# Optimization experiments

Hardware: AMD Instinct MI355X
Metric: run time of the kernel (lower is better)

Reference implementation:

```python
import jax, jax.numpy as jnp
import numpy as np

B, C, T = 8, 1025, 3000


def setup_inputs() -> dict:
    key = jax.random.key(0)
    k1, k2 = jax.random.split(key)
    x_real = jax.random.normal(k1, (B, C, T), dtype=jnp.float32)
    x_imag = jax.random.normal(k2, (B, C, T), dtype=jnp.float32)
    return {"x_real": x_real, "x_imag": x_imag}


def reference(x_real, x_imag):
    # coherent_polar: magnitude + min-max-normalized unwrapped phase, cat on channel dim
    magnitude = jnp.sqrt(x_real * x_real + x_imag * x_imag)  # torch.abs(complex)
    phase = jnp.arctan2(x_imag, x_real)                      # torch.angle

    pi = jnp.float32(np.pi)
    two_pi = jnp.float32(2.0 * np.pi)

    phase_diff = phase[:, :, 1:] - phase[:, :, :-1]          # [B, C, T-1]
    # per-step correction: +2pi where diff < -pi, -2pi where diff > pi
    steps = jnp.where(phase_diff < -pi, two_pi, jnp.float32(0.0)) \
          + jnp.where(phase_diff > pi, -two_pi, jnp.float32(0.0))
    # the original sequential loop is an inclusive prefix-sum of the steps
    correction = jnp.concatenate(
        [jnp.zeros_like(phase[:, :, :1]), jnp.cumsum(steps, axis=2)], axis=2
    )  # [B, C, T]

    unwrapped = phase + correction
    phase_min = jnp.min(unwrapped, axis=2, keepdims=True)
    phase_max = jnp.max(unwrapped, axis=2, keepdims=True)
    phase_norm = (unwrapped - phase_min) / (phase_max - phase_min + 1e-8)

    return jnp.concatenate([magnitude, phase_norm], axis=1)  # [B, 2C, T]
```

## Files before the change

### kernel.cpp

```cpp
#include <hip/hip_runtime.h>

namespace {
constexpr int kB = 8;
constexpr int kC = 1025;
constexpr int kT = 3000;
constexpr int kThreads = 256;
constexpr int kWaves = kThreads / 64;
constexpr int kSeg = kThreads * 4;
constexpr int kNSeg = 3;
constexpr float kPi = 3.14159265358979323846f;
constexpr float kTwoPi = 6.28318530717958647692f;
constexpr float kPiO2 = 1.57079632679489661923f;
}

typedef float v4f __attribute__((ext_vector_type(4)));
typedef float v2f __attribute__((ext_vector_type(2)));

__device__ __forceinline__ v2f atan_core2(v2f t) {
  const v2f s = t * t;
  v2f p = v2f{0.00282363896258175373f, 0.00282363896258175373f};
  p = p * s + v2f{-0.0159569028764963150f, -0.0159569028764963150f};
  p = p * s + v2f{0.0425049886107444763f, 0.0425049886107444763f};
  p = p * s + v2f{-0.0748900920152664185f, -0.0748900920152664185f};
  p = p * s + v2f{0.106347933411598206f, 0.106347933411598206f};
  p = p * s + v2f{-0.142027363181114197f, -0.142027363181114197f};
  p = p * s + v2f{0.199926957488059998f, 0.199926957488059998f};
  p = p * s + v2f{-0.333331018686294556f, -0.333331018686294556f};
  return (p * s) * t + t;
}

__device__ __forceinline__ void fast_atan2_4(const v4f y4, const v4f x4,
                                             float out[4]) {
  float t[4], ax[4], ay[4];
  const float xs[4] = {x4.x, x4.y, x4.z, x4.w};
  const float ys[4] = {y4.x, y4.y, y4.z, y4.w};
#pragma unroll
  for (int k = 0; k < 4; ++k) {
    ax[k] = __builtin_fabsf(xs[k]);
    ay[k] = __builtin_fabsf(ys[k]);
    const float mx = fmaxf(ax[k], ay[k]);
    const float mn = fminf(ax[k], ay[k]);
    float tt = mn * __builtin_amdgcn_rcpf(mx);
    if (mx == 0.0f) tt = 0.0f;
    t[k] = tt;
  }
  const v2f a01 = atan_core2(v2f{t[0], t[1]});
  const v2f a23 = atan_core2(v2f{t[2], t[3]});
  const float av[4] = {a01.x, a01.y, a23.x, a23.y};
#pragma unroll
  for (int k = 0; k < 4; ++k) {
    float a = av[k];
    a = (ay[k] > ax[k]) ? (kPiO2 - a) : a;
    a = (xs[k] < 0.0f) ? (kPi - a) : a;
    out[k] = copysignf(a, ys[k]);
  }
}

__global__ __launch_bounds__(kThreads, 8) void coherent_polar_kernel(
    const float* __restrict__ xr, const float* __restrict__ xi,
    float* __restrict__ out) {
  __shared__ float s_last[kNSeg][kThreads];
  __shared__ float s_wsum[kWaves][kNSeg];
  __shared__ float s_wmin[kWaves][kNSeg];
  __shared__ float s_wmax[kWaves][kNSeg];

  const int row = blockIdx.x;
  const int b = row / kC;
  const int c = row - b * kC;
  const float* re = xr + (size_t)row * kT;
  const float* im = xi + (size_t)row * kT;
  float* mag_out = out + ((size_t)b * (2 * kC) + c) * kT;
  float* ph_out  = out + ((size_t)b * (2 * kC) + kC + c) * kT;

  const int tid = threadIdx.x;
  const int lane = tid & 63;
  const int wave = tid >> 6;

  bool act[kNSeg];
  int offs[kNSeg];
#pragma unroll
  for (int s = 0; s < kNSeg; ++s) {
    offs[s] = s * kSeg + tid * 4;
    act[s] = offs[s] < kT;
  }

  v4f r4[kNSeg], i4[kNSeg];
#pragma unroll
  for (int s = 0; s < kNSeg; ++s) {
    if (act[s]) {
      r4[s] = *reinterpret_cast<const v4f*>(re + offs[s]);
      i4[s] = *reinterpret_cast<const v4f*>(im + offs[s]);
    }
  }

  float ph[kNSeg][4];
#pragma unroll
  for (int s = 0; s < kNSeg; ++s) {
    if (act[s]) {
      v4f m4;
      m4.x = __builtin_amdgcn_sqrtf(fmaf(r4[s].x, r4[s].x, i4[s].x * i4[s].x));
      m4.y = __builtin_amdgcn_sqrtf(fmaf(r4[s].y, r4[s].y, i4[s].y * i4[s].y));
      m4.z = __builtin_amdgcn_sqrtf(fmaf(r4[s].z, r4[s].z, i4[s].z * i4[s].z));
      m4.w = __builtin_amdgcn_sqrtf(fmaf(r4[s].w, r4[s].w, i4[s].w * i4[s].w));
      *reinterpret_cast<v4f*>(mag_out + offs[s]) = m4;
      fast_atan2_4(i4[s], r4[s], ph[s]);
    }
  }

#pragma unroll
  for (int s = 0; s < kNSeg; ++s) s_last[s][tid] = act[s] ? ph[s][3] : 0.0f;
  __syncthreads();
  float prevph[kNSeg];
#pragma unroll
  for (int s = 0; s < kNSeg; ++s) {
    if (tid > 0)       prevph[s] = s_last[s][tid - 1];
    else if (s > 0)    prevph[s] = s_last[s - 1][kThreads - 1];
    else               prevph[s] = ph[0][0];
  }

  float T[kNSeg];
#pragma unroll
  for (int s = 0; s < kNSeg; ++s) {
    float run = 0.0f;
    if (act[s]) {
      float p = prevph[s];
#pragma unroll
      for (int k = 0; k < 4; ++k) {
        const float cur = ph[s][k];
        const float d = cur - p;
        p = cur;
        float step = 0.0f;
        if (d < -kPi) step = kTwoPi;
        else if (d > kPi) step = -kTwoPi;
        run += step;
        ph[s][k] = cur + run;
      }
    }
    T[s] = act[s] ? run : 0.0f;
  }

  float inc[kNSeg] = {T[0], T[1], T[2]};
#pragma unroll
  for (int d = 1; d < 64; d <<= 1) {
#pragma unroll
    for (int s = 0; s < kNSeg; ++s) {
      const float n = __shfl_up(inc[s], d);
      if (lane >= d) inc[s] += n;
    }
  }
  float excl[kNSeg];
#pragma unroll
  for (int s = 0; s < kNSeg; ++s) excl[s] = inc[s] - T[s];

  float mn[kNSeg], mx[kNSeg];
#pragma unroll
  for (int s = 0; s < kNSeg; ++s) {
    mn[s] = __builtin_inff();
    mx[s] = -__builtin_inff();
    if (act[s]) {
#pragma unroll
      for (int k = 0; k < 4; ++k) {
        const float u = ph[s][k] + excl[s];
        mn[s] = fminf(mn[s], u);
        mx[s] = fmaxf(mx[s], u);
      }
    }
  }
#pragma unroll
  for (int m = 32; m >= 1; m >>= 1) {
#pragma unroll
    for (int s = 0; s < kNSeg; ++s) {
      mn[s] = fminf(mn[s], __shfl_xor(mn[s], m));
      mx[s] = fmaxf(mx[s], __shfl_xor(mx[s], m));
    }
  }
  if (lane == 63) {
#pragma unroll
    for (int s = 0; s < kNSeg; ++s) s_wsum[wave][s] = inc[s];
  }
  if (lane == 0) {
#pragma unroll
    for (int s = 0; s < kNSeg; ++s) { s_wmin[wave][s] = mn[s]; s_wmax[wave][s] = mx[s]; }
  }
  __syncthreads();

  float wavePref[kWaves][kNSeg];
  float blockTot[kNSeg];
#pragma unroll
  for (int s = 0; s < kNSeg; ++s) {
    float acc = 0.0f;
#pragma unroll
    for (int w = 0; w < kWaves; ++w) { wavePref[w][s] = acc; acc += s_wsum[w][s]; }
    blockTot[s] = acc;
  }
  float segBase[kNSeg];
  segBase[0] = 0.0f;
  segBase[1] = blockTot[0];
  segBase[2] = blockTot[0] + blockTot[1];

  float gmn = __builtin_inff();
  float gmx = -__builtin_inff();
#pragma unroll
  for (int w = 0; w < kWaves; ++w) {
#pragma unroll
    for (int s = 0; s < kNSeg; ++s) {
      const float off = segBase[s] + wavePref[w][s];
      gmn = fminf(gmn, s_wmin[w][s] + off);
      gmx = fmaxf(gmx, s_wmax[w][s] + off);
    }
  }
  const float inv = 1.0f / (gmx - gmn + 1e-8f);

#pragma unroll
  for (int s = 0; s < kNSeg; ++s) {
    if (act[s]) {
      const float base = segBase[s] + wavePref[wave][s] + excl[s] - gmn;
      v4f o;
      o.x = (ph[s][0] + base) * inv;
      o.y = (ph[s][1] + base) * inv;
      o.z = (ph[s][2] + base) * inv;
      o.w = (ph[s][3] + base) * inv;
      *reinterpret_cast<v4f*>(ph_out + offs[s]) = o;
    }
  }
}

extern "C" void kernel_launch(void* const* d_in, const int* in_sizes, int n_in,
                              void* d_out, int out_size, void* d_ws, size_t ws_size,
                              hipStream_t stream) {
  const float* xr = (const float*)d_in[0];
  const float* xi = (const float*)d_in[1];
  float* out = (float*)d_out;
  coherent_polar_kernel<<<dim3(kB * kC), dim3(kThreads), 0, stream>>>(xr, xi, out);
}
```

Baseline: 80.21 us.

## Process four rows per block with register prefetch of next row

Switches from one block per row to a grid of 2050 blocks, each looping over four rows with a stride of 2050. The next row's real and imaginary data is loaded into registers while the current row's scan and normalization run, so global loads overlap with compute. Output stores become nontemporal, and __syncthreads is replaced by a custom LDS wait plus barrier. The costs are higher register pressure, reflected in launch bounds lowered from 8 to 4 blocks, and fewer concurrent blocks.

```diff
diff --git a/kernel.cpp b/kernel.cpp
--- a/kernel.cpp
+++ b/kernel.cpp
@@ -3,11 +3,14 @@
 namespace {
 constexpr int kB = 8;
 constexpr int kC = 1025;
+constexpr int kRows = kB * kC;
 constexpr int kT = 3000;
 constexpr int kThreads = 256;
 constexpr int kWaves = kThreads / 64;
 constexpr int kSeg = kThreads * 4;
 constexpr int kNSeg = 3;
+constexpr int kGridB = 2050;
+constexpr int kRowsPer = 4;
 constexpr float kPi = 3.14159265358979323846f;
 constexpr float kTwoPi = 6.28318530717958647692f;
 constexpr float kPiO2 = 1.57079632679489661923f;
@@ -15,6 +18,12 @@
 
 typedef float v4f __attribute__((ext_vector_type(4)));
 typedef float v2f __attribute__((ext_vector_type(2)));
+
+__device__ __forceinline__ void sync_lds() {
+  asm volatile("s_waitcnt lgkmcnt(0)" ::: "memory");
+  __builtin_amdgcn_s_barrier();
+  asm volatile("" ::: "memory");
+}
 
 __device__ __forceinline__ v2f atan_core2(v2f t) {
   const v2f s = t * t;
@@ -56,7 +65,20 @@
   }
 }
 
-__global__ __launch_bounds__(kThreads, 8) void coherent_polar_kernel(
+__device__ __forceinline__ void load_row(const float* __restrict__ re,
+                                         const float* __restrict__ im,
+                                         int tid, v4f r4[kNSeg], v4f i4[kNSeg]) {
+#pragma unroll
+  for (int s = 0; s < kNSeg; ++s) {
+    const int off = s * kSeg + tid * 4;
+    if (s < 2 || off < kT) {
+      r4[s] = *reinterpret_cast<const v4f*>(re + off);
+      i4[s] = *reinterpret_cast<const v4f*>(im + off);
+    }
+  }
+}
+
+__global__ __launch_bounds__(kThreads, 4) void coherent_polar_kernel(
     const float* __restrict__ xr, const float* __restrict__ xi,
     float* __restrict__ out) {
   __shared__ float s_last[kNSeg][kThreads];
@@ -64,163 +86,163 @@
   __shared__ float s_wmin[kWaves][kNSeg];
   __shared__ float s_wmax[kWaves][kNSeg];
 
-  const int row = blockIdx.x;
-  const int b = row / kC;
-  const int c = row - b * kC;
-  const float* re = xr + (size_t)row * kT;
-  const float* im = xi + (size_t)row * kT;
-  float* mag_out = out + ((size_t)b * (2 * kC) + c) * kT;
-  float* ph_out  = out + ((size_t)b * (2 * kC) + kC + c) * kT;
-
+  const int bid = blockIdx.x;
   const int tid = threadIdx.x;
   const int lane = tid & 63;
   const int wave = tid >> 6;
-
-  bool act[kNSeg];
-  int offs[kNSeg];
-#pragma unroll
-  for (int s = 0; s < kNSeg; ++s) {
-    offs[s] = s * kSeg + tid * 4;
-    act[s] = offs[s] < kT;
-  }
-
-  v4f r4[kNSeg], i4[kNSeg];
-#pragma unroll
-  for (int s = 0; s < kNSeg; ++s) {
-    if (act[s]) {
-      r4[s] = *reinterpret_cast<const v4f*>(re + offs[s]);
-      i4[s] = *reinterpret_cast<const v4f*>(im + offs[s]);
-    }
-  }
-
-  float ph[kNSeg][4];
-#pragma unroll
-  for (int s = 0; s < kNSeg; ++s) {
-    if (act[s]) {
-      v4f m4;
-      m4.x = __builtin_amdgcn_sqrtf(fmaf(r4[s].x, r4[s].x, i4[s].x * i4[s].x));
-      m4.y = __builtin_amdgcn_sqrtf(fmaf(r4[s].y, r4[s].y, i4[s].y * i4[s].y));
-      m4.z = __builtin_amdgcn_sqrtf(fmaf(r4[s].z, r4[s].z, i4[s].z * i4[s].z));
-      m4.w = __builtin_amdgcn_sqrtf(fmaf(r4[s].w, r4[s].w, i4[s].w * i4[s].w));
-      *reinterpret_cast<v4f*>(mag_out + offs[s]) = m4;
-      fast_atan2_4(i4[s], r4[s], ph[s]);
-    }
-  }
-
-#pragma unroll
-  for (int s = 0; s < kNSeg; ++s) s_last[s][tid] = act[s] ? ph[s][3] : 0.0f;
-  __syncthreads();
-  float prevph[kNSeg];
-#pragma unroll
-  for (int s = 0; s < kNSeg; ++s) {
-    if (tid > 0)       prevph[s] = s_last[s][tid - 1];
-    else if (s > 0)    prevph[s] = s_last[s - 1][kThreads - 1];
-    else               prevph[s] = ph[0][0];
-  }
-
-  float T[kNSeg];
-#pragma unroll
-  for (int s = 0; s < kNSeg; ++s) {
-    float run = 0.0f;
-    if (act[s]) {
-      float p = prevph[s];
-#pragma unroll
-      for (int k = 0; k < 4; ++k) {
-        const float cur = ph[s][k];
-        const float d = cur - p;
-        p = cur;
-        float step = 0.0f;
-        if (d < -kPi) step = kTwoPi;
-        else if (d > kPi) step = -kTwoPi;
-        run += step;
-        ph[s][k] = cur + run;
-      }
-    }
-    T[s] = act[s] ? run : 0.0f;
-  }
-
-  float inc[kNSeg] = {T[0], T[1], T[2]};
-#pragma unroll
-  for (int d = 1; d < 64; d <<= 1) {
-#pragma unroll
-    for (int s = 0; s < kNSeg; ++s) {
-      const float n = __shfl_up(inc[s], d);
-      if (lane >= d) inc[s] += n;
-    }
-  }
-  float excl[kNSeg];
-#pragma unroll
-  for (int s = 0; s < kNSeg; ++s) excl[s] = inc[s] - T[s];
-
-  float mn[kNSeg], mx[kNSeg];
-#pragma unroll
-  for (int s = 0; s < kNSeg; ++s) {
-    mn[s] = __builtin_inff();
-    mx[s] = -__builtin_inff();
-    if (act[s]) {
-#pragma unroll
-      for (int k = 0; k < 4; ++k) {
-        const float u = ph[s][k] + excl[s];
-        mn[s] = fminf(mn[s], u);
-        mx[s] = fmaxf(mx[s], u);
-      }
-    }
-  }
-#pragma unroll
-  for (int m = 32; m >= 1; m >>= 1) {
-#pragma unroll
-    for (int s = 0; s < kNSeg; ++s) {
-      mn[s] = fminf(mn[s], __shfl_xor(mn[s], m));
-      mx[s] = fmaxf(mx[s], __shfl_xor(mx[s], m));
-    }
-  }
-  if (lane == 63) {
-#pragma unroll
-    for (int s = 0; s < kNSeg; ++s) s_wsum[wave][s] = inc[s];
-  }
-  if (lane == 0) {
-#pragma unroll
-    for (int s = 0; s < kNSeg; ++s) { s_wmin[wave][s] = mn[s]; s_wmax[wave][s] = mx[s]; }
-  }
-  __syncthreads();
-
-  float wavePref[kWaves][kNSeg];
-  float blockTot[kNSeg];
-#pragma unroll
-  for (int s = 0; s < kNSeg; ++s) {
-    float acc = 0.0f;
-#pragma unroll
-    for (int w = 0; w < kWaves; ++w) { wavePref[w][s] = acc; acc += s_wsum[w][s]; }
-    blockTot[s] = acc;
-  }
-  float segBase[kNSeg];
-  segBase[0] = 0.0f;
-  segBase[1] = blockTot[0];
-  segBase[2] = blockTot[0] + blockTot[1];
-
-  float gmn = __builtin_inff();
-  float gmx = -__builtin_inff();
-#pragma unroll
-  for (int w = 0; w < kWaves; ++w) {
-#pragma unroll
-    for (int s = 0; s < kNSeg; ++s) {
-      const float off = segBase[s] + wavePref[w][s];
-      gmn = fminf(gmn, s_wmin[w][s] + off);
-      gmx = fmaxf(gmx, s_wmax[w][s] + off);
-    }
-  }
-  const float inv = 1.0f / (gmx - gmn + 1e-8f);
-
-#pragma unroll
-  for (int s = 0; s < kNSeg; ++s) {
-    if (act[s]) {
-      const float base = segBase[s] + wavePref[wave][s] + excl[s] - gmn;
-      v4f o;
-      o.x = (ph[s][0] + base) * inv;
-      o.y = (ph[s][1] + base) * inv;
-      o.z = (ph[s][2] + base) * inv;
-      o.w = (ph[s][3] + base) * inv;
-      *reinterpret_cast<v4f*>(ph_out + offs[s]) = o;
+  const bool act2 = tid * 4 + 2 * kSeg < kT;
+
+  v4f r4[kNSeg], i4[kNSeg], r4n[kNSeg], i4n[kNSeg];
+  load_row(xr + (size_t)bid * kT, xi + (size_t)bid * kT, tid, r4, i4);
+
+#pragma unroll 1
+  for (int r = 0; r < kRowsPer; ++r) {
+    const int row = bid + r * kGridB;
+    const int b = row / kC;
+    const int c = row - b * kC;
+    float* mag_out = out + ((size_t)b * (2 * kC) + c) * kT;
+    float* ph_out  = out + ((size_t)b * (2 * kC) + kC + c) * kT;
+
+    float ph[kNSeg][4];
+#pragma unroll
+    for (int s = 0; s < kNSeg; ++s) {
+      if (s < 2 || act2) {
+        v4f m4;
+        m4.x = __builtin_amdgcn_sqrtf(fmaf(r4[s].x, r4[s].x, i4[s].x * i4[s].x));
+        m4.y = __builtin_amdgcn_sqrtf(fmaf(r4[s].y, r4[s].y, i4[s].y * i4[s].y));
+        m4.z = __builtin_amdgcn_sqrtf(fmaf(r4[s].z, r4[s].z, i4[s].z * i4[s].z));
+        m4.w = __builtin_amdgcn_sqrtf(fmaf(r4[s].w, r4[s].w, i4[s].w * i4[s].w));
+        __builtin_nontemporal_store(m4, reinterpret_cast<v4f*>(mag_out + s * kSeg + tid * 4));
+        fast_atan2_4(i4[s], r4[s], ph[s]);
+      }
+    }
+
+    if (r + 1 < kRowsPer) {
+      const int nrow = row + kGridB;
+      load_row(xr + (size_t)nrow * kT, xi + (size_t)nrow * kT, tid, r4n, i4n);
+    }
+
+#pragma unroll
+    for (int s = 0; s < kNSeg; ++s)
+      s_last[s][tid] = (s < 2 || act2) ? ph[s][3] : 0.0f;
+    sync_lds();
+    float prevph[kNSeg];
+#pragma unroll
+    for (int s = 0; s < kNSeg; ++s) {
+      if (tid > 0)       prevph[s] = s_last[s][tid - 1];
+      else if (s > 0)    prevph[s] = s_last[s - 1][kThreads - 1];
+      else               prevph[s] = ph[0][0];
+    }
+
+    float T[kNSeg];
+#pragma unroll
+    for (int s = 0; s < kNSeg; ++s) {
+      float run = 0.0f;
+      if (s < 2 || act2) {
+        float p = prevph[s];
+#pragma unroll
+        for (int k = 0; k < 4; ++k) {
+          const float cur = ph[s][k];
+          const float d = cur - p;
+          p = cur;
+          float step = 0.0f;
+          if (d < -kPi) step = kTwoPi;
+          else if (d > kPi) step = -kTwoPi;
+          run += step;
+          ph[s][k] = cur + run;
+        }
+      }
+      T[s] = (s < 2 || act2) ? run : 0.0f;
+    }
+
+    float inc[kNSeg] = {T[0], T[1], T[2]};
+#pragma unroll
+    for (int d = 1; d < 64; d <<= 1) {
+#pragma unroll
+      for (int s = 0; s < kNSeg; ++s) {
+        const float n = __shfl_up(inc[s], d);
+        if (lane >= d) inc[s] += n;
+      }
+    }
+    float excl[kNSeg];
+#pragma unroll
+    for (int s = 0; s < kNSeg; ++s) excl[s] = inc[s] - T[s];
+
+    float mn[kNSeg], mx[kNSeg];
+#pragma unroll
+    for (int s = 0; s < kNSeg; ++s) {
+      mn[s] = __builtin_inff();
+      mx[s] = -__builtin_inff();
+      if (s < 2 || act2) {
+#pragma unroll
+        for (int k = 0; k < 4; ++k) {
+          const float u = ph[s][k] + excl[s];
+          mn[s] = fminf(mn[s], u);
+          mx[s] = fmaxf(mx[s], u);
+        }
+      }
+    }
+#pragma unroll
+    for (int m = 32; m >= 1; m >>= 1) {
+#pragma unroll
+      for (int s = 0; s < kNSeg; ++s) {
+        mn[s] = fminf(mn[s], __shfl_xor(mn[s], m));
+        mx[s] = fmaxf(mx[s], __shfl_xor(mx[s], m));
+      }
+    }
+    if (lane == 63) {
+#pragma unroll
+      for (int s = 0; s < kNSeg; ++s) s_wsum[wave][s] = inc[s];
+    }
+    if (lane == 0) {
+#pragma unroll
+      for (int s = 0; s < kNSeg; ++s) { s_wmin[wave][s] = mn[s]; s_wmax[wave][s] = mx[s]; }
+    }
+    sync_lds();
+
+    float wavePref[kWaves][kNSeg];
+    float blockTot[kNSeg];
+#pragma unroll
+    for (int s = 0; s < kNSeg; ++s) {
+      float acc = 0.0f;
+#pragma unroll
+      for (int w = 0; w < kWaves; ++w) { wavePref[w][s] = acc; acc += s_wsum[w][s]; }
+      blockTot[s] = acc;
+    }
+    float segBase[kNSeg];
+    segBase[0] = 0.0f;
+    segBase[1] = blockTot[0];
+    segBase[2] = blockTot[0] + blockTot[1];
+
+    float gmn = __builtin_inff();
+    float gmx = -__builtin_inff();
+#pragma unroll
+    for (int w = 0; w < kWaves; ++w) {
+#pragma unroll
+      for (int s = 0; s < kNSeg; ++s) {
+        const float off = segBase[s] + wavePref[w][s];
+        gmn = fminf(gmn, s_wmin[w][s] + off);
+        gmx = fmaxf(gmx, s_wmax[w][s] + off);
+      }
+    }
+    const float inv = 1.0f / (gmx - gmn + 1e-8f);
+
+#pragma unroll
+    for (int s = 0; s < kNSeg; ++s) {
+      if (s < 2 || act2) {
+        const float base = segBase[s] + wavePref[wave][s] + excl[s] - gmn;
+        v4f o;
+        o.x = (ph[s][0] + base) * inv;
+        o.y = (ph[s][1] + base) * inv;
+        o.z = (ph[s][2] + base) * inv;
+        o.w = (ph[s][3] + base) * inv;
+        __builtin_nontemporal_store(o, reinterpret_cast<v4f*>(ph_out + s * kSeg + tid * 4));
+      }
+    }
+
+    if (r + 1 < kRowsPer) {
+#pragma unroll
+      for (int s = 0; s < kNSeg; ++s) { r4[s] = r4n[s]; i4[s] = i4n[s]; }
     }
   }
 }
@@ -231,5 +253,5 @@
   const float* xr = (const float*)d_in[0];
   const float* xi = (const float*)d_in[1];
   float* out = (float*)d_out;
-  coherent_polar_kernel<<<dim3(kB * kC), dim3(kThreads), 0, stream>>>(xr, xi, out);
-}
+  coherent_polar_kernel<<<dim3(kGridB), dim3(kThreads), 0, stream>>>(xr, xi, out);
+}
```

Result: faster. 70.18 us (-12.5%).
